# Optimization experiments

Hardware: AMD Instinct MI355X
Metric: run time of the kernel (lower is better)

Reference implementation:

```python
import jax, jax.numpy as jnp
import numpy as np

B, T, C = 2, 2048, 1024
NH, NKV, HD = 16, 4, 64
VEC = 32  # ve_gate_channels


def _rope(x, cos, sin):
    d = x.shape[-1] // 2
    x1, x2 = x[..., :d], x[..., d:]
    return jnp.concatenate([x1 * cos + x2 * sin, -x1 * sin + x2 * cos], axis=-1)


def _rmsnorm(x):
    eps = jnp.finfo(x.dtype).eps
    return x * jax.lax.rsqrt(jnp.mean(x * x, axis=-1, keepdims=True) + eps)


def setup_inputs() -> dict:
    key = jax.random.key(0)
    ks = jax.random.split(key, 9)
    s = 0.02
    return {
        "x": jax.random.normal(ks[0], (B, T, C), jnp.float32),
        "ve": jax.random.normal(ks[1], (B, T, NKV * HD), jnp.float32),
        "cos": jax.random.normal(ks[2], (1, T, 1, HD // 2), jnp.float32),
        "sin": jax.random.normal(ks[3], (1, T, 1, HD // 2), jnp.float32),
        "Wq": jax.random.normal(ks[4], (C, NH * HD), jnp.float32) * s,
        "Wk": jax.random.normal(ks[5], (C, NKV * HD), jnp.float32) * s,
        "Wv": jax.random.normal(ks[6], (C, NKV * HD), jnp.float32) * s,
        "Wproj": jax.random.normal(ks[7], (C, C), jnp.float32) * s,
        "Wgate": jax.random.normal(ks[8], (VEC, NKV), jnp.float32) * s,
        "window_size": 1024,
    }


def reference(x, ve, cos, sin, Wq, Wk, Wv, Wproj, Wgate, window_size):
    Bx, Tx, Cx = x.shape
    q = (x @ Wq).reshape(Bx, Tx, NH, HD)
    k = (x @ Wk).reshape(Bx, Tx, NKV, HD)
    v = (x @ Wv).reshape(Bx, Tx, NKV, HD)

    # value-embedding gate (has_ve True for this layer)
    gate = 2.0 * jax.nn.sigmoid(x[..., :VEC] @ Wgate)  # [B,T,NKV]
    v = v + gate[..., None] * ve.reshape(Bx, Tx, NKV, HD)

    q, k = _rope(q, cos, sin), _rope(k, cos, sin)
    q, k = _rmsnorm(q), _rmsnorm(k)

    q = q.transpose(0, 2, 1, 3)  # [B,NH,T,HD]
    k = k.transpose(0, 2, 1, 3)  # [B,NKV,T,HD]
    v = v.transpose(0, 2, 1, 3)

    # GQA: each KV head serves NH//NKV consecutive q heads
    g = NH // NKV
    k = jnp.repeat(k, g, axis=1)
    v = jnp.repeat(v, g, axis=1)

    row = jnp.arange(Tx)[:, None]
    col = jnp.arange(Tx)[None, :]
    mask = (col <= row) & (col >= row - window_size)  # causal sliding window

    scores = jnp.einsum("bhqd,bhkd->bhqk", q, k) / np.sqrt(HD).astype(np.float32)
    scores = jnp.where(mask[None, None], scores, jnp.finfo(scores.dtype).min)
    attn = jax.nn.softmax(scores, axis=-1)
    y = jnp.einsum("bhqk,bhkd->bhqd", attn, v)

    y = y.transpose(0, 2, 1, 3).reshape(Bx, Tx, Cx)
    return y @ Wproj
```

## Files before the change

### kernel.cpp

```cpp
#include <hip/hip_runtime.h>

typedef __bf16 bf16x8 __attribute__((ext_vector_type(8)));
typedef __bf16 bf16x4 __attribute__((ext_vector_type(4)));
typedef float f32x4 __attribute__((ext_vector_type(4)));

__device__ inline float tof(float v) { return v; }
__device__ inline float tof(__bf16 v) { return (float)v; }

__device__ inline bf16x8 load8(const __bf16* p) { return *(const bf16x8*)p; }
__device__ inline bf16x8 load8(const float* p) {
    const float4 a = *(const float4*)p;
    const float4 b = *(const float4*)(p + 4);
    bf16x8 r;
    r[0] = (__bf16)a.x; r[1] = (__bf16)a.y; r[2] = (__bf16)a.z; r[3] = (__bf16)a.w;
    r[4] = (__bf16)b.x; r[5] = (__bf16)b.y; r[6] = (__bf16)b.z; r[7] = (__bf16)b.w;
    return r;
}

__device__ __forceinline__ void cp16(__bf16* lds, const __bf16* g) {
    __builtin_amdgcn_global_load_lds((__attribute__((address_space(1))) void*)g,
                                     (__attribute__((address_space(3))) void*)lds,
                                     16, 0, 0);
}

__global__ void sniff_kernel(const unsigned short* __restrict__ xs, int* flag) {
    int tid = threadIdx.x;
    int bad = 0;
    for (int i = tid; i < 512; i += 64) {
        unsigned int f = ((unsigned int)xs[i]) << 16;
        float v = __uint_as_float(f);
        float a = fabsf(v);
        if (!(a <= 1e4f) || (a != 0.f && a < 1e-6f)) bad++;
    }
    bad += __shfl_xor(bad, 1);  bad += __shfl_xor(bad, 2);
    bad += __shfl_xor(bad, 4);  bad += __shfl_xor(bad, 8);
    bad += __shfl_xor(bad, 16); bad += __shfl_xor(bad, 32);
    if (tid == 0) *flag = (bad > 32) ? 1 : 0;
}

template <typename T>
__device__ __forceinline__ void prep_body(
    const T* __restrict__ x, const T* __restrict__ ve,
    const T* __restrict__ cosp, const T* __restrict__ sinp,
    const T* __restrict__ Wq, const T* __restrict__ Wk,
    const T* __restrict__ Wv, const T* __restrict__ Wp, const T* __restrict__ Wg,
    __bf16* __restrict__ xb, __bf16* __restrict__ veb,
    float* __restrict__ cosf_, float* __restrict__ sinf_,
    __bf16* __restrict__ WqT, __bf16* __restrict__ WkT,
    __bf16* __restrict__ WvT, __bf16* __restrict__ WpT,
    __bf16* __restrict__ wgb, __bf16* tile)
{
    const int b = blockIdx.x, tid = threadIdx.x;

    if (b < 2625) {
        int g = b * 256 + tid;
        if (g < 524288) {
            *(bf16x8*)(xb + (size_t)g * 8) = load8(x + (size_t)g * 8);
        } else if (g < 655360) {
            int gg = g - 524288;
            *(bf16x8*)(veb + (size_t)gg * 8) = load8(ve + (size_t)gg * 8);
        } else if (g < 663552) {
            int gg = g - 655360;
            const T* s = cosp + (size_t)gg * 8; float* d = cosf_ + (size_t)gg * 8;
#pragma unroll
            for (int j = 0; j < 8; ++j) d[j] = tof(s[j]);
        } else if (g < 671744) {
            int gg = g - 663552;
            const T* s = sinp + (size_t)gg * 8; float* d = sinf_ + (size_t)gg * 8;
#pragma unroll
            for (int j = 0; j < 8; ++j) d[j] = tof(s[j]);
        } else if (g < 671760) {
            int gg = g - 671744;
            const T* s = Wg + (size_t)gg * 8; __bf16* d = wgb + (size_t)gg * 8;
#pragma unroll
            for (int j = 0; j < 8; ++j) d[j] = (__bf16)tof(s[j]);
        }
    } else {
        int idx = b - 2625;
        const T* src; __bf16* dst; int C;
        if (idx < 256)      { src = Wq; dst = WqT; C = 1024; }
        else if (idx < 320) { src = Wk; dst = WkT; C = 256;  idx -= 256; }
        else if (idx < 384) { src = Wv; dst = WvT; C = 256;  idx -= 320; }
        else                { src = Wp; dst = WpT; C = 1024; idx -= 384; }
        const int ctiles = C >> 6;
        const int r0 = (idx / ctiles) * 64, c0 = (idx % ctiles) * 64;
#pragma unroll
        for (int i = 0; i < 2; ++i) {
            int c = tid + i * 256, ir = c >> 3, ic = (c & 7) * 8;
            *(bf16x8*)(&tile[ir * 72 + ic]) = load8(src + (size_t)(r0 + ir) * C + c0 + ic);
        }
        __syncthreads();
#pragma unroll
        for (int i = 0; i < 2; ++i) {
            int c = tid + i * 256, orr = c >> 3, okc = (c & 7) * 8;
            bf16x8 v;
#pragma unroll
            for (int j = 0; j < 8; ++j) v[j] = tile[(okc + j) * 72 + orr];
            *(bf16x8*)(dst + (size_t)(c0 + orr) * 1024 + r0 + okc) = v;
        }
    }
}

__global__ __launch_bounds__(256) void prep_kernel(
    const void* x, const void* ve, const void* cosp, const void* sinp,
    const void* Wq, const void* Wk, const void* Wv, const void* Wp, const void* Wg,
    __bf16* xb, __bf16* veb, float* cosf_, float* sinf_,
    __bf16* WqT, __bf16* WkT, __bf16* WvT, __bf16* WpT,
    __bf16* wgb, const int* __restrict__ flag)
{
    __shared__ __bf16 tile[64 * 72];
    if (*flag) {
        prep_body<float>((const float*)x, (const float*)ve, (const float*)cosp,
                         (const float*)sinp, (const float*)Wq, (const float*)Wk,
                         (const float*)Wv, (const float*)Wp, (const float*)Wg,
                         xb, veb, cosf_, sinf_, WqT, WkT, WvT, WpT, wgb, tile);
    } else {
        prep_body<__bf16>((const __bf16*)x, (const __bf16*)ve, (const __bf16*)cosp,
                          (const __bf16*)sinp, (const __bf16*)Wq, (const __bf16*)Wk,
                          (const __bf16*)Wv, (const __bf16*)Wp, (const __bf16*)Wg,
                          xb, veb, cosf_, sinf_, WqT, WkT, WvT, WpT, wgb, tile);
    }
}

__global__ __launch_bounds__(256) void qkv_kernel(
    const __bf16* __restrict__ xb,
    const __bf16* __restrict__ WqT, const __bf16* __restrict__ WkT,
    const __bf16* __restrict__ WvT, const __bf16* __restrict__ veb,
    const float* __restrict__ cosf_, const float* __restrict__ sinf_,
    const __bf16* __restrict__ wgb,
    __bf16* __restrict__ qo, __bf16* __restrict__ ko, __bf16* __restrict__ vTo)
{
    const int row0 = blockIdx.x * 128;
    const int cb = blockIdx.y;
    const __bf16* BT; int col0, mode;
    if (cb < 8)       { BT = WqT; col0 = cb * 128;        mode = 0; }
    else if (cb < 10) { BT = WkT; col0 = (cb - 8) * 128;  mode = 1; }
    else              { BT = WvT; col0 = (cb - 10) * 128; mode = 2; }

    __shared__ __align__(16) __bf16 As[128 * 32];
    __shared__ __align__(16) __bf16 Bs[128 * 32];

    const int tid  = threadIdx.x;
    const int w    = tid >> 6;
    const int lane = tid & 63;
    const int quad = lane >> 4;
    const int l15  = lane & 15;
    const int wr   = (w >> 1) * 64, wc = (w & 1) * 64;
    const int h    = (col0 + wc) >> 6;

    f32x4 acc[4][4];
#pragma unroll
    for (int mi = 0; mi < 4; ++mi)
#pragma unroll
        for (int nj = 0; nj < 4; ++nj) acc[mi][nj] = (f32x4){0.f, 0.f, 0.f, 0.f};

    bf16x8 wgB;
#pragma unroll
    for (int j = 0; j < 8; ++j) wgB[j] = (__bf16)0.f;
    if (mode == 2 && l15 < 4) {
#pragma unroll
        for (int j = 0; j < 8; ++j) wgB[j] = wgb[(quad * 8 + j) * 4 + l15];
    }
    f32x4 zacc[4];
#pragma unroll
    for (int mi = 0; mi < 4; ++mi) zacc[mi] = (f32x4){0.f, 0.f, 0.f, 0.f};

    for (int kk = 0; kk < 1024; kk += 32) {
#pragma unroll
        for (int i = 0; i < 2; ++i) {
            int c = i * 256 + (w << 6) + lane;
            int rr = c >> 2, kc = (c & 3) << 3;
            cp16(&As[c << 3], &xb[(size_t)(row0 + rr) * 1024 + kk + kc]);
            cp16(&Bs[c << 3], &BT[(size_t)(col0 + rr) * 1024 + kk + kc]);
        }
        __syncthreads();
        bf16x8 a[4], bfr[4];
#pragma unroll
        for (int mi = 0; mi < 4; ++mi) a[mi]  = *(const bf16x8*)(&As[(wr + mi * 16 + l15) * 32 + quad * 8]);
#pragma unroll
        for (int nj = 0; nj < 4; ++nj) bfr[nj] = *(const bf16x8*)(&Bs[(wc + nj * 16 + l15) * 32 + quad * 8]);
        if (mode == 2 && kk == 0) {
#pragma unroll
            for (int mi = 0; mi < 4; ++mi)
                zacc[mi] = __builtin_amdgcn_mfma_f32_16x16x32_bf16(a[mi], wgB, zacc[mi], 0, 0, 0);
        }
#pragma unroll
        for (int mi = 0; mi < 4; ++mi)
#pragma unroll
            for (int nj = 0; nj < 4; ++nj)
                acc[mi][nj] = __builtin_amdgcn_mfma_f32_16x16x32_bf16(a[mi], bfr[nj], acc[mi][nj], 0, 0, 0);
        __syncthreads();
    }

    if (mode < 2) {
        __bf16* dst = (mode == 0) ? qo : ko;
        const int nh = (mode == 0) ? 16 : 4;
#pragma unroll
        for (int mi = 0; mi < 4; ++mi) {
#pragma unroll
            for (int r = 0; r < 4; ++r) {
                int row = row0 + wr + mi * 16 + quad * 4 + r;
                int b = row >> 11, t = row & 2047;
                float c0 = cosf_[t * 32 + l15];
                float c1 = cosf_[t * 32 + 16 + l15];
                float s0 = sinf_[t * 32 + l15];
                float s1 = sinf_[t * 32 + 16 + l15];
                float v0 =  c0 * acc[mi][0][r] + s0 * acc[mi][2][r];
                float v1 =  c1 * acc[mi][1][r] + s1 * acc[mi][3][r];
                float v2 = -s0 * acc[mi][0][r] + c0 * acc[mi][2][r];
                float v3 = -s1 * acc[mi][1][r] + c1 * acc[mi][3][r];
                float ss = v0 * v0 + v1 * v1 + v2 * v2 + v3 * v3;
                ss += __shfl_xor(ss, 1); ss += __shfl_xor(ss, 2);
                ss += __shfl_xor(ss, 4); ss += __shfl_xor(ss, 8);
                float sc = rsqrtf(ss * (1.f / 64.f) + 1.1920929e-7f);
                size_t base = (((size_t)b * nh + h) * 2048 + t) * 64;
                dst[base + 0 * 16 + l15] = (__bf16)(v0 * sc);
                dst[base + 1 * 16 + l15] = (__bf16)(v1 * sc);
                dst[base + 2 * 16 + l15] = (__bf16)(v2 * sc);
                dst[base + 3 * 16 + l15] = (__bf16)(v3 * sc);
            }
        }
    } else {
#pragma unroll
        for (int mi = 0; mi < 4; ++mi) {
            int rowb = row0 + wr + mi * 16 + quad * 4;
            int b = rowb >> 11, t0 = rowb & 2047;
            float gg[4];
#pragma unroll
            for (int r = 0; r < 4; ++r) {
                float zv = __shfl(zacc[mi][r], quad * 16 + h);
                gg[r] = 2.f / (1.f + __expf(-zv));
            }
#pragma unroll
            for (int nj = 0; nj < 4; ++nj) {
                int d = nj * 16 + l15;
                bf16x4 pack;
#pragma unroll
                for (int r = 0; r < 4; ++r) {
                    int row = rowb + r;
                    float val = acc[mi][nj][r] + gg[r] * tof(veb[(size_t)row * 256 + h * 64 + d]);
                    pack[r] = (__bf16)val;
                }
                size_t a = (((size_t)b * 4 + h) * 64 + d) * 2048 + t0;
                *(bf16x4*)(&vTo[a]) = pack;
            }
        }
    }
}

__global__ __launch_bounds__(256) void attn_kernel(
    const __bf16* __restrict__ qg, const __bf16* __restrict__ kg,
    const __bf16* __restrict__ vTg, __bf16* __restrict__ yo,
    const int* __restrict__ winp)
{
    const int q0 = blockIdx.x * 128;
    const int hh = blockIdx.y, b = blockIdx.z;
    const int kvh = hh >> 2;
    const int W = winp[0];

    const int tid  = threadIdx.x;
    const int w    = tid >> 6;
    const int lane = tid & 63;
    const int quad = lane >> 4;
    const int l15  = lane & 15;

    __shared__ __align__(16) __bf16 Ks[2][64 * 64];
    __shared__ __align__(16) __bf16 Vt[2][64 * 64];
    __shared__ __align__(16) __bf16 Ps[4][32 * 72];

    bf16x8 qf[2][2];
#pragma unroll
    for (int i = 0; i < 2; ++i) {
        size_t qb = (((size_t)b * 16 + hh) * 2048 + q0 + w * 32 + i * 16 + l15) * 64;
        qf[i][0] = *(const bf16x8*)(&qg[qb + quad * 8]);
        qf[i][1] = *(const bf16x8*)(&qg[qb + 32 + quad * 8]);
    }

    f32x4 oacc[2][4];
    float lsum[2][4];
#pragma unroll
    for (int i = 0; i < 2; ++i)
#pragma unroll
        for (int n = 0; n < 4; ++n) {
            oacc[i][n] = (f32x4){0.f, 0.f, 0.f, 0.f};
            lsum[i][n] = 0.f;
        }

    const int lo = q0 - W;
    const int kt_lo = lo > 0 ? (lo >> 6) : 0;
    const int kt_hi = (q0 + 127) >> 6;
    const size_t kvbase = ((size_t)b * 4 + kvh) * 2048 * 64;

    auto stage = [&](int buf, int k0) {
#pragma unroll
        for (int i = 0; i < 2; ++i) {
            int c = i * 256 + tid;
            int rr = c >> 3;
            int jj = (c & 7) ^ (rr & 7);
            cp16(&Ks[buf][c * 8], &kg[kvbase + (size_t)(k0 + rr) * 64 + jj * 8]);
            cp16(&Vt[buf][c * 8], &vTg[kvbase + (size_t)rr * 2048 + k0 + jj * 8]);
        }
    };

    stage(0, kt_lo * 64);
    __syncthreads();

    int cur = 0;
    for (int kt = kt_lo; kt <= kt_hi; ++kt) {
        const int k0 = kt * 64;
        const bool need_mask = (k0 + 63 > q0) || (q0 + 127 - k0 > W);
        if (kt < kt_hi) stage(cur ^ 1, k0 + 64);

        f32x4 sacc[2][4];
#pragma unroll
        for (int i = 0; i < 2; ++i)
#pragma unroll
            for (int n = 0; n < 4; ++n) sacc[i][n] = (f32x4){0.f, 0.f, 0.f, 0.f};
        const __bf16* Kc = &Ks[cur][0];
#pragma unroll
        for (int n = 0; n < 4; ++n) {
            int m = n * 16 + l15;
            bf16x8 b0 = *(const bf16x8*)(&Kc[m * 64 + (quad ^ (m & 7)) * 8]);
            bf16x8 b1 = *(const bf16x8*)(&Kc[m * 64 + ((4 + quad) ^ (m & 7)) * 8]);
#pragma unroll
            for (int i = 0; i < 2; ++i) {
                sacc[i][n] = __builtin_amdgcn_mfma_f32_16x16x32_bf16(qf[i][0], b0, sacc[i][n], 0, 0, 0);
                sacc[i][n] = __builtin_amdgcn_mfma_f32_16x16x32_bf16(qf[i][1], b1, sacc[i][n], 0, 0, 0);
            }
        }

#pragma unroll
        for (int i = 0; i < 2; ++i) {
#pragma unroll
            for (int r = 0; r < 4; ++r) {
                const int row_g = q0 + w * 32 + i * 16 + quad * 4 + r;
#pragma unroll
                for (int n = 0; n < 4; ++n) {
                    float p = exp2f(fmaf(sacc[i][n][r], 0.18033688f, -11.5415603f));
                    if (need_mask) {
                        int col_g = k0 + n * 16 + l15;
                        bool ok = (col_g <= row_g) && (row_g - col_g <= W);
                        p = ok ? p : 0.f;
                    }
                    lsum[i][r] += p;
                    Ps[w][(i * 16 + quad * 4 + r) * 72 + n * 16 + l15] = (__bf16)p;
                }
            }
        }
        asm volatile("s_waitcnt lgkmcnt(0)" ::: "memory");

        const __bf16* Vc = &Vt[cur][0];
#pragma unroll
        for (int ks = 0; ks < 2; ++ks) {
            bf16x8 pfr0 = *(const bf16x8*)(&Ps[w][l15 * 72 + ks * 32 + quad * 8]);
            bf16x8 pfr1 = *(const bf16x8*)(&Ps[w][(16 + l15) * 72 + ks * 32 + quad * 8]);
#pragma unroll
            for (int n = 0; n < 4; ++n) {
                int m = n * 16 + l15;
                bf16x8 bv = *(const bf16x8*)(&Vc[m * 64 + ((ks * 4 + quad) ^ (m & 7)) * 8]);
                oacc[0][n] = __builtin_amdgcn_mfma_f32_16x16x32_bf16(pfr0, bv, oacc[0][n], 0, 0, 0);
                oacc[1][n] = __builtin_amdgcn_mfma_f32_16x16x32_bf16(pfr1, bv, oacc[1][n], 0, 0, 0);
            }
        }

        __syncthreads();
        cur ^= 1;
    }

#pragma unroll
    for (int i = 0; i < 2; ++i) {
#pragma unroll
        for (int r = 0; r < 4; ++r) {
            float l = lsum[i][r];
            l += __shfl_xor(l, 1); l += __shfl_xor(l, 2);
            l += __shfl_xor(l, 4); l += __shfl_xor(l, 8);
            float inv = 1.f / l;
            int t = q0 + w * 32 + i * 16 + quad * 4 + r;
            size_t base = ((size_t)(b * 2048 + t)) * 1024 + hh * 64;
#pragma unroll
            for (int n = 0; n < 4; ++n)
                yo[base + n * 16 + l15] = (__bf16)(oacc[i][n][r] * inv);
        }
    }
}

__global__ __launch_bounds__(256) void proj_kernel(
    const __bf16* __restrict__ y, const __bf16* __restrict__ WpT,
    void* __restrict__ outp, const int* __restrict__ flag)
{
    const int isf32 = *flag;
    const int row0 = blockIdx.x * 128;
    const int col0 = blockIdx.y * 64;
    __shared__ __align__(16) __bf16 As[128 * 32];
    __shared__ __align__(16) __bf16 Bs[64 * 32];

    const int tid  = threadIdx.x;
    const int w    = tid >> 6;
    const int lane = tid & 63;
    const int quad = lane >> 4;
    const int l15  = lane & 15;
    const int wr   = w * 32;

    f32x4 acc[2][4];
#pragma unroll
    for (int mi = 0; mi < 2; ++mi)
#pragma unroll
        for (int nj = 0; nj < 4; ++nj) acc[mi][nj] = (f32x4){0.f, 0.f, 0.f, 0.f};

    for (int kk = 0; kk < 1024; kk += 32) {
#pragma unroll
        for (int i = 0; i < 2; ++i) {
            int c = i * 256 + (w << 6) + lane;
            int rr = c >> 2, kc = (c & 3) << 3;
            cp16(&As[c << 3], &y[(size_t)(row0 + rr) * 1024 + kk + kc]);
        }
        {
            int c = (w << 6) + lane;
            int rr = c >> 2, kc = (c & 3) << 3;
            cp16(&Bs[c << 3], &WpT[(size_t)(col0 + rr) * 1024 + kk + kc]);
        }
        __syncthreads();
        bf16x8 a[2], bfr[4];
#pragma unroll
        for (int mi = 0; mi < 2; ++mi) a[mi]  = *(const bf16x8*)(&As[(wr + mi * 16 + l15) * 32 + quad * 8]);
#pragma unroll
        for (int nj = 0; nj < 4; ++nj) bfr[nj] = *(const bf16x8*)(&Bs[(nj * 16 + l15) * 32 + quad * 8]);
#pragma unroll
        for (int mi = 0; mi < 2; ++mi)
#pragma unroll
            for (int nj = 0; nj < 4; ++nj)
                acc[mi][nj] = __builtin_amdgcn_mfma_f32_16x16x32_bf16(a[mi], bfr[nj], acc[mi][nj], 0, 0, 0);
        __syncthreads();
    }

#pragma unroll
    for (int mi = 0; mi < 2; ++mi)
#pragma unroll
        for (int r = 0; r < 4; ++r) {
            int row = row0 + wr + mi * 16 + quad * 4 + r;
            if (isf32) {
                float* out = (float*)outp;
#pragma unroll
                for (int nj = 0; nj < 4; ++nj)
                    out[(size_t)row * 1024 + col0 + nj * 16 + l15] = acc[mi][nj][r];
            } else {
                __bf16* out = (__bf16*)outp;
#pragma unroll
                for (int nj = 0; nj < 4; ++nj)
                    out[(size_t)row * 1024 + col0 + nj * 16 + l15] = (__bf16)acc[mi][nj][r];
            }
        }
}

extern "C" void kernel_launch(void* const* d_in, const int* in_sizes, int n_in,
                              void* d_out, int out_size, void* d_ws, size_t ws_size,
                              hipStream_t stream) {
    const int* win = (const int*)d_in[9];

    char* p = (char*)d_ws;
    int*    flag = (int*)p;                    p += 256;
    __bf16* q_ws = (__bf16*)p;                 p += (size_t)4194304 * 2;
    __bf16* k_ws = (__bf16*)p;                 p += (size_t)1048576 * 2;
    __bf16* vT_ws= (__bf16*)p;                 p += (size_t)1048576 * 2;
    __bf16* y_ws = (__bf16*)p;                 p += (size_t)4194304 * 2;
    __bf16* xb   = (__bf16*)p;                 p += (size_t)4194304 * 2;
    __bf16* veb  = (__bf16*)p;                 p += (size_t)1048576 * 2;
    __bf16* WqT  = (__bf16*)p;                 p += (size_t)1048576 * 2;
    __bf16* WkT  = (__bf16*)p;                 p += (size_t)262144 * 2;
    __bf16* WvT  = (__bf16*)p;                 p += (size_t)262144 * 2;
    __bf16* WpT  = (__bf16*)p;                 p += (size_t)1048576 * 2;
    float*  cosf_ = (float*)p;                 p += (size_t)65536 * 4;
    float*  sinf_ = (float*)p;                 p += (size_t)65536 * 4;
    __bf16* wgb   = (__bf16*)p;                p += 256;

    sniff_kernel<<<1, 64, 0, stream>>>((const unsigned short*)d_in[0], flag);

    prep_kernel<<<3265, 256, 0, stream>>>(
        d_in[0], d_in[1], d_in[2], d_in[3], d_in[4], d_in[5], d_in[6], d_in[7],
        d_in[8], xb, veb, cosf_, sinf_, WqT, WkT, WvT, WpT, wgb, flag);

    qkv_kernel<<<dim3(32, 12), 256, 0, stream>>>(xb, WqT, WkT, WvT, veb,
                                                 cosf_, sinf_, wgb, q_ws, k_ws, vT_ws);

    attn_kernel<<<dim3(16, 16, 2), 256, 0, stream>>>(q_ws, k_ws, vT_ws, y_ws, win);

    proj_kernel<<<dim3(32, 16), 256, 0, stream>>>(y_ws, WpT, d_out, flag);
}
```

Baseline: 198.6 us.

## Double-buffer LDS staging in QKV and projection GEMMs, shrink QKV tiles

```diff
diff --git a/kernel.cpp b/kernel.cpp
--- a/kernel.cpp
+++ b/kernel.cpp
@@ -132,25 +132,24 @@
 {
     const int row0 = blockIdx.x * 128;
     const int cb = blockIdx.y;
-    const __bf16* BT; int col0, mode;
-    if (cb < 8)       { BT = WqT; col0 = cb * 128;        mode = 0; }
-    else if (cb < 10) { BT = WkT; col0 = (cb - 8) * 128;  mode = 1; }
-    else              { BT = WvT; col0 = (cb - 10) * 128; mode = 2; }
-
-    __shared__ __align__(16) __bf16 As[128 * 32];
-    __shared__ __align__(16) __bf16 Bs[128 * 32];
+    const __bf16* BT; int col0, h, mode;
+    if (cb < 16)      { BT = WqT; col0 = cb * 64;        h = cb;      mode = 0; }
+    else if (cb < 20) { BT = WkT; col0 = (cb - 16) * 64; h = cb - 16; mode = 1; }
+    else              { BT = WvT; col0 = (cb - 20) * 64; h = cb - 20; mode = 2; }
+
+    __shared__ __align__(16) __bf16 As[2][128 * 32];
+    __shared__ __align__(16) __bf16 Bs[2][64 * 32];
 
     const int tid  = threadIdx.x;
     const int w    = tid >> 6;
     const int lane = tid & 63;
     const int quad = lane >> 4;
     const int l15  = lane & 15;
-    const int wr   = (w >> 1) * 64, wc = (w & 1) * 64;
-    const int h    = (col0 + wc) >> 6;
-
-    f32x4 acc[4][4];
-#pragma unroll
-    for (int mi = 0; mi < 4; ++mi)
+    const int wr   = w * 32;
+
+    f32x4 acc[2][4];
+#pragma unroll
+    for (int mi = 0; mi < 2; ++mi)
 #pragma unroll
         for (int nj = 0; nj < 4; ++nj) acc[mi][nj] = (f32x4){0.f, 0.f, 0.f, 0.f};
 
@@ -161,31 +160,37 @@
 #pragma unroll
         for (int j = 0; j < 8; ++j) wgB[j] = wgb[(quad * 8 + j) * 4 + l15];
     }
-    f32x4 zacc[4];
-#pragma unroll
-    for (int mi = 0; mi < 4; ++mi) zacc[mi] = (f32x4){0.f, 0.f, 0.f, 0.f};
+    f32x4 zacc[2];
+    zacc[0] = (f32x4){0.f, 0.f, 0.f, 0.f};
+    zacc[1] = (f32x4){0.f, 0.f, 0.f, 0.f};
+
+    auto stage = [&](int buf, int kk) {
+#pragma unroll
+        for (int i = 0; i < 2; ++i) {
+            int c = i * 256 + tid;
+            cp16(&As[buf][c * 8], &xb[(size_t)(row0 + (c >> 2)) * 1024 + kk + ((c & 3) << 3)]);
+        }
+        cp16(&Bs[buf][tid * 8], &BT[(size_t)(col0 + (tid >> 2)) * 1024 + kk + ((tid & 3) << 3)]);
+    };
+
+    stage(0, 0);
+    __syncthreads();
 
     for (int kk = 0; kk < 1024; kk += 32) {
-#pragma unroll
-        for (int i = 0; i < 2; ++i) {
-            int c = i * 256 + (w << 6) + lane;
-            int rr = c >> 2, kc = (c & 3) << 3;
-            cp16(&As[c << 3], &xb[(size_t)(row0 + rr) * 1024 + kk + kc]);
-            cp16(&Bs[c << 3], &BT[(size_t)(col0 + rr) * 1024 + kk + kc]);
-        }
-        __syncthreads();
-        bf16x8 a[4], bfr[4];
-#pragma unroll
-        for (int mi = 0; mi < 4; ++mi) a[mi]  = *(const bf16x8*)(&As[(wr + mi * 16 + l15) * 32 + quad * 8]);
-#pragma unroll
-        for (int nj = 0; nj < 4; ++nj) bfr[nj] = *(const bf16x8*)(&Bs[(wc + nj * 16 + l15) * 32 + quad * 8]);
+        const int cur = (kk >> 5) & 1;
+        if (kk + 32 < 1024) stage(cur ^ 1, kk + 32);
+
+        bf16x8 a[2], bfr[4];
+#pragma unroll
+        for (int mi = 0; mi < 2; ++mi) a[mi]  = *(const bf16x8*)(&As[cur][(wr + mi * 16 + l15) * 32 + quad * 8]);
+#pragma unroll
+        for (int nj = 0; nj < 4; ++nj) bfr[nj] = *(const bf16x8*)(&Bs[cur][(nj * 16 + l15) * 32 + quad * 8]);
         if (mode == 2 && kk == 0) {
-#pragma unroll
-            for (int mi = 0; mi < 4; ++mi)
-                zacc[mi] = __builtin_amdgcn_mfma_f32_16x16x32_bf16(a[mi], wgB, zacc[mi], 0, 0, 0);
-        }
-#pragma unroll
-        for (int mi = 0; mi < 4; ++mi)
+            zacc[0] = __builtin_amdgcn_mfma_f32_16x16x32_bf16(a[0], wgB, zacc[0], 0, 0, 0);
+            zacc[1] = __builtin_amdgcn_mfma_f32_16x16x32_bf16(a[1], wgB, zacc[1], 0, 0, 0);
+        }
+#pragma unroll
+        for (int mi = 0; mi < 2; ++mi)
 #pragma unroll
             for (int nj = 0; nj < 4; ++nj)
                 acc[mi][nj] = __builtin_amdgcn_mfma_f32_16x16x32_bf16(a[mi], bfr[nj], acc[mi][nj], 0, 0, 0);
@@ -196,7 +201,7 @@
         __bf16* dst = (mode == 0) ? qo : ko;
         const int nh = (mode == 0) ? 16 : 4;
 #pragma unroll
-        for (int mi = 0; mi < 4; ++mi) {
+        for (int mi = 0; mi < 2; ++mi) {
 #pragma unroll
             for (int r = 0; r < 4; ++r) {
                 int row = row0 + wr + mi * 16 + quad * 4 + r;
@@ -222,7 +227,7 @@
         }
     } else {
 #pragma unroll
-        for (int mi = 0; mi < 4; ++mi) {
+        for (int mi = 0; mi < 2; ++mi) {
             int rowb = row0 + wr + mi * 16 + quad * 4;
             int b = rowb >> 11, t0 = rowb & 2047;
             float gg[4];
@@ -391,8 +396,8 @@
     const int isf32 = *flag;
     const int row0 = blockIdx.x * 128;
     const int col0 = blockIdx.y * 64;
-    __shared__ __align__(16) __bf16 As[128 * 32];
-    __shared__ __align__(16) __bf16 Bs[64 * 32];
+    __shared__ __align__(16) __bf16 As[2][128 * 32];
+    __shared__ __align__(16) __bf16 Bs[2][64 * 32];
 
     const int tid  = threadIdx.x;
     const int w    = tid >> 6;
@@ -407,24 +412,27 @@
 #pragma unroll
         for (int nj = 0; nj < 4; ++nj) acc[mi][nj] = (f32x4){0.f, 0.f, 0.f, 0.f};
 
+    auto stage = [&](int buf, int kk) {
+#pragma unroll
+        for (int i = 0; i < 2; ++i) {
+            int c = i * 256 + tid;
+            cp16(&As[buf][c * 8], &y[(size_t)(row0 + (c >> 2)) * 1024 + kk + ((c & 3) << 3)]);
+        }
+        cp16(&Bs[buf][tid * 8], &WpT[(size_t)(col0 + (tid >> 2)) * 1024 + kk + ((tid & 3) << 3)]);
+    };
+
+    stage(0, 0);
+    __syncthreads();
+
     for (int kk = 0; kk < 1024; kk += 32) {
-#pragma unroll
-        for (int i = 0; i < 2; ++i) {
-            int c = i * 256 + (w << 6) + lane;
-            int rr = c >> 2, kc = (c & 3) << 3;
-            cp16(&As[c << 3], &y[(size_t)(row0 + rr) * 1024 + kk + kc]);
-        }
-        {
-            int c = (w << 6) + lane;
-            int rr = c >> 2, kc = (c & 3) << 3;
-            cp16(&Bs[c << 3], &WpT[(size_t)(col0 + rr) * 1024 + kk + kc]);
-        }
-        __syncthreads();
+        const int cur = (kk >> 5) & 1;
+        if (kk + 32 < 1024) stage(cur ^ 1, kk + 32);
+
         bf16x8 a[2], bfr[4];
 #pragma unroll
-        for (int mi = 0; mi < 2; ++mi) a[mi]  = *(const bf16x8*)(&As[(wr + mi * 16 + l15) * 32 + quad * 8]);
-#pragma unroll
-        for (int nj = 0; nj < 4; ++nj) bfr[nj] = *(const bf16x8*)(&Bs[(nj * 16 + l15) * 32 + quad * 8]);
+        for (int mi = 0; mi < 2; ++mi) a[mi]  = *(const bf16x8*)(&As[cur][(wr + mi * 16 + l15) * 32 + quad * 8]);
+#pragma unroll
+        for (int nj = 0; nj < 4; ++nj) bfr[nj] = *(const bf16x8*)(&Bs[cur][(nj * 16 + l15) * 32 + quad * 8]);
 #pragma unroll
         for (int mi = 0; mi < 2; ++mi)
 #pragma unroll
@@ -479,7 +487,7 @@
         d_in[0], d_in[1], d_in[2], d_in[3], d_in[4], d_in[5], d_in[6], d_in[7],
         d_in[8], xb, veb, cosf_, sinf_, WqT, WkT, WvT, WpT, wgb, flag);
 
-    qkv_kernel<<<dim3(32, 12), 256, 0, stream>>>(xb, WqT, WkT, WvT, veb,
+    qkv_kernel<<<dim3(32, 24), 256, 0, stream>>>(xb, WqT, WkT, WvT, veb,
                                                  cosf_, sinf_, wgb, q_ws, k_ws, vT_ws);
 
     attn_kernel<<<dim3(16, 16, 2), 256, 0, stream>>>(q_ws, k_ws, vT_ws, y_ws, win);
```

After: 201.0 us. About the same (+1.2%).
